# Kernel optimization log

Hardware: AMD Instinct MI355X
Metric: run time of the kernel (lower is better)

The kernel has to match this reference:

```python
import jax, jax.numpy as jnp
import numpy as np

D = 12  # grid size per axis (self.shape = [12,12,12])
BN_EPS = 1e-5


def _scatter(feats, idx, B):
    # feats: [N, C], idx: [N, 4] = (b, z, y, x). Coords are unique -> .set is exact.
    g = jnp.zeros((B, D, D, D, feats.shape[-1]), feats.dtype)
    return g.at[idx[:, 0], idx[:, 1], idx[:, 2], idx[:, 3]].set(feats)


def _subm_conv_bn_relu(feats, idx, B, W, b, gamma, beta):
    # Submanifold 3x3x3 conv == dense SAME conv on zero-filled grid, restricted
    # to the active sites (inactive neighbors contribute zero features).
    g = _scatter(feats, idx, B)  # [B, D, D, D, Cin]
    y = jax.lax.conv_general_dilated(
        g, W, window_strides=(1, 1, 1), padding='SAME',
        dimension_numbers=('NDHWC', 'DHWIO', 'NDHWC')) + b
    f = y[idx[:, 0], idx[:, 1], idx[:, 2], idx[:, 3]]  # gather active -> [N, Cout]
    # BatchNorm1d (training mode): biased batch stats over the N active points.
    mu = f.mean(axis=0)
    var = f.var(axis=0)
    f = (f - mu) * jax.lax.rsqrt(var + BN_EPS) * gamma + beta
    return jax.nn.relu(f)


def setup_inputs() -> dict:
    key = jax.random.key(0)
    B, per, Cin = 512, 864, 16
    N = B * per
    k_feat, k_coord, kp = jax.random.split(key, 3)
    # unique active voxels per batch element
    pkeys = jax.random.split(k_coord, B)
    lin = jax.vmap(lambda k: jax.random.permutation(k, D * D * D))(pkeys)[:, :per]  # [B, per]
    z, y, x = lin // (D * D), (lin // D) % D, lin % D
    bids = jnp.broadcast_to(jnp.arange(B)[:, None], (B, per))
    indices = jnp.stack([bids, z, y, x], axis=-1).reshape(N, 4).astype(jnp.int32)
    features = jax.random.normal(k_feat, (N, Cin), dtype=jnp.float32)
    ks = jax.random.split(kp, 6)
    inp = {
        'features': features, 'indices': indices, 'batch_size': B,
        'W0': jax.random.normal(ks[0], (3, 3, 3, Cin, 64), jnp.float32) * 0.05,
        'b0': jax.random.normal(ks[1], (64,), jnp.float32) * 0.05,
        'gamma0': jnp.ones((64,), jnp.float32), 'beta0': jnp.zeros((64,), jnp.float32),
        'W1': jax.random.normal(ks[2], (3, 3, 3, 64, 128), jnp.float32) * 0.05,
        'b1': jax.random.normal(ks[3], (128,), jnp.float32) * 0.05,
        'gamma1': jnp.ones((128,), jnp.float32), 'beta1': jnp.zeros((128,), jnp.float32),
        'W2': jax.random.normal(ks[4], (3, 3, 3, 128, 64), jnp.float32) * 0.05,
        'b2': jax.random.normal(ks[5], (64,), jnp.float32) * 0.05,
        'gamma2': jnp.ones((64,), jnp.float32), 'beta2': jnp.zeros((64,), jnp.float32),
    }
    return inp


def reference(features, indices, batch_size, W0, b0, gamma0, beta0,
              W1, b1, gamma1, beta1, W2, b2, gamma2, beta2):
    B = int(batch_size)
    f = _subm_conv_bn_relu(features, indices, B, W0, b0, gamma0, beta0)
    f = _subm_conv_bn_relu(f, indices, B, W1, b1, gamma1, beta1)
    f = _subm_conv_bn_relu(f, indices, B, W2, b2, gamma2, beta2)
    g = _scatter(f, indices, B)                 # [B, D, D, D, Cout]
    return jnp.transpose(g, (0, 4, 1, 2, 3))    # spconv .dense(): [B, C, D, H, W]
```

## Files before the change

### kernel.cpp

```cpp
#include <hip/hip_runtime.h>

#define DD 12
#define VOX 1728
#define BN_EPS 1e-5f
#define BATCH 512
#define PER 864
#define PERZ 865
#define NTOT (BATCH * PER)

typedef __attribute__((ext_vector_type(8))) short short8;
typedef __attribute__((ext_vector_type(4))) float f32x4;
typedef unsigned short u16;

__device__ inline u16 f2b(float f) {
    union { float f; unsigned u; } v; v.f = f;
    unsigned r = v.u + 0x7fffu + ((v.u >> 16) & 1u);
    return (u16)(r >> 16);
}
__device__ inline float b2f(u16 h) {
    union { unsigned u; float f; } v; v.u = ((unsigned)h) << 16;
    return v.f;
}
constexpr int ilog2(int v) { return v == 1 ? 0 : 1 + ilog2(v / 2); }

__device__ __forceinline__ void async_copy16(const void* g, void* l) {
    __builtin_amdgcn_global_load_lds(
        (const __attribute__((address_space(1))) void*)g,
        (__attribute__((address_space(3))) void*)l, 16, 0, 0);
}

template<int N> __device__ __forceinline__ void wait_vm() {
    if constexpr (N == 0)       asm volatile("s_waitcnt vmcnt(0)"  ::: "memory");
    else if constexpr (N == 8)  asm volatile("s_waitcnt vmcnt(8)"  ::: "memory");
    else if constexpr (N == 10) asm volatile("s_waitcnt vmcnt(10)" ::: "memory");
    else if constexpr (N == 12) asm volatile("s_waitcnt vmcnt(12)" ::: "memory");
    else if constexpr (N == 18) asm volatile("s_waitcnt vmcnt(18)" ::: "memory");
    else static_assert(N == 0, "unhandled vmcnt value");
}

__global__ void build_map_kernel(const int* __restrict__ idx, int* __restrict__ map, int N) {
    int p = blockIdx.x * blockDim.x + threadIdx.x;
    if (p >= N) return;
    const int4 v = ((const int4*)idx)[p];
    map[v.x * VOX + (v.y * DD + v.z) * DD + v.w] = p;
}

__global__ void build_nbr_kernel(const int* __restrict__ idx, const int* __restrict__ map,
                                 u16* __restrict__ nbr, int N) {
    int p = blockIdx.x * blockDim.x + threadIdx.x;
    if (p >= N) return;
    const int4 v = ((const int4*)idx)[p];
    const int base = v.x * VOX;
    const int lb = v.x * PER;
    #pragma unroll
    for (int nk = 0; nk < 27; nk++) {
        int dz = nk / 9 - 1, dy = (nk / 3) % 3 - 1, dx = nk % 3 - 1;
        int zz = v.y + dz, yy = v.z + dy, xx = v.w + dx;
        u16 out = PER;
        if (zz >= 0 && zz < DD && yy >= 0 && yy < DD && xx >= 0 && xx < DD) {
            int q = map[base + (zz * DD + yy) * DD + xx];
            if (q >= 0) out = (u16)(q - lb);
        }
        nbr[nk * N + p] = out;
    }
    #pragma unroll
    for (int nk = 27; nk < 32; nk++) nbr[nk * N + p] = PER;
}

__global__ void transpose_w_kernel(const float* __restrict__ W, u16* __restrict__ Wt,
                                   int K, int COUT, int Kpad) {
    int i = blockIdx.x * blockDim.x + threadIdx.x;
    if (i >= K * COUT) return;
    int n = i % COUT, k = i / COUT;
    Wt[(size_t)n * Kpad + k] = f2b(W[i]);
}

__global__ void cast_bf16_kernel(const float* __restrict__ in, u16* __restrict__ out, int total4) {
    int i = blockIdx.x * blockDim.x + threadIdx.x;
    if (i >= total4) return;
    int p = i >> 2, c4 = i & 3;
    int b = p / PERZ, r = p - b * PERZ;
    ushort4 o = make_ushort4(0, 0, 0, 0);
    if (r < PER) {
        float4 v = ((const float4*)in)[(size_t)(b * PER + r) * 4 + c4];
        o.x = f2b(v.x); o.y = f2b(v.y); o.z = f2b(v.z); o.w = f2b(v.w);
    }
    ((ushort4*)out)[i] = o;
}

template<int CIN, int COUT, int BM, int WM, int WN>
__global__ __launch_bounds__(256) void conv_mfma_kernel(
    const u16* __restrict__ fin, const u16* __restrict__ nbr, const u16* __restrict__ Wt,
    const float* __restrict__ bias, float* __restrict__ y, float* __restrict__ stats) {
    constexpr int Kpad   = (27 * CIN + 63) & ~63;
    constexpr int KSTEPS = Kpad / 64;
    constexpr int L2C    = ilog2(CIN);
    constexpr int BN     = WN * 64;
    constexpr int ASLOTS = BM / 32;
    constexpr int BSLOTS = BN / 32;
    constexpr int A_OFF  = BN * 128;
    constexpr int BUFB   = (BM + BN) * 128;
    static_assert(KSTEPS >= 3, "pipeline prologue needs >=3 K-steps");
    __shared__ char smem[2 * BUFB];

    const int perx = gridDim.x >> 3;
    const int bid = (blockIdx.x & 7) * perx + (blockIdx.x >> 3);
    const int p0 = bid * BM;

    const int tid = threadIdx.x;
    const int wave = tid >> 6, lane = tid & 63;
    const int wm = wave / WN, wn = wave % WN;
    const int lq = lane >> 4, lr = lane & 15;
    const int lrow = lane >> 3;
    const int kc_d = (lane & 7) ^ (lrow & 7);

    int qvoff[ASLOTS], gbase[ASLOTS];
    #pragma unroll
    for (int i = 0; i < ASLOTS; i++) {
        int m = (wave * ASLOTS + i) * 8 + lrow;
        int p = p0 + m;
        int b = p / PER;
        qvoff[i] = (((kc_d * 8) >> L2C) * NTOT + p) * 2;
        gbase[i] = b * PERZ * CIN + ((kc_d * 8) & (CIN - 1));
    }
    int bvoff[BSLOTS];
    #pragma unroll
    for (int j = 0; j < BSLOTS; j++)
        bvoff[j] = ((wave * BSLOTS + j) * 8 + lrow) * Kpad + kc_d * 8;

    int phs[2];
    phs[0] = ((0 + lq) ^ (lr & 7)) * 16;
    phs[1] = ((4 + lq) ^ (lr & 7)) * 16;
    const int aBase = A_OFF + (wm * 64 + lr) * 128;
    const int bBase = (wn * 64 + lr) * 128;

    const f32x4 fzero = {0.f, 0.f, 0.f, 0.f};
    f32x4 acc[4][4];
    #pragma unroll
    for (int i = 0; i < 4; i++)
        #pragma unroll
        for (int j = 0; j < 4; j++) acc[i][j] = fzero;

    u16 q[ASLOTS];
    auto loadQ = [&](int step) {
        int sQ = ((step * 64) >> L2C) * (NTOT * 2);
        #pragma unroll
        for (int i = 0; i < ASLOTS; i++)
            q[i] = *(const u16*)((const char*)nbr + qvoff[i] + sQ);
    };
    auto stage = [&](int step, int bo) {
        int sG = (step * 64) & (CIN - 1);
        const u16* fs = fin + sG;
        #pragma unroll
        for (int i = 0; i < ASLOTS; i++)
            async_copy16(fs + gbase[i] + ((int)q[i] << L2C),
                         smem + bo + A_OFF + (wave * ASLOTS + i) * 1024);
        const u16* wsrc = Wt + step * 64;
        #pragma unroll
        for (int j = 0; j < BSLOTS; j++)
            async_copy16(wsrc + bvoff[j], smem + bo + (wave * BSLOTS + j) * 1024);
    };

    loadQ(0);
    stage(0, 0);
    loadQ(1);

    #pragma unroll 1
    for (int kb = 0; kb < KSTEPS; kb++) {
        if (kb + 1 < KSTEPS) {
            stage(kb + 1, ((kb + 1) & 1) * BUFB);
            if (kb + 2 < KSTEPS) {
                loadQ(kb + 2);
                wait_vm<2 * ASLOTS + BSLOTS>();
            } else {
                wait_vm<ASLOTS + BSLOTS>();
            }
        } else {
            wait_vm<0>();
        }
        __builtin_amdgcn_s_barrier();

        const int so = (kb & 1) * BUFB;
        __builtin_amdgcn_s_setprio(1);
        #pragma unroll
        for (int s = 0; s < 2; s++) {
            short8 af[4], bfr[4];
            #pragma unroll
            for (int i = 0; i < 4; i++)
                af[i] = *(const short8*)(smem + so + aBase + i * 2048 + phs[s]);
            #pragma unroll
            for (int j = 0; j < 4; j++)
                bfr[j] = *(const short8*)(smem + so + bBase + j * 2048 + phs[s]);
            #pragma unroll
            for (int i = 0; i < 4; i++)
                #pragma unroll
                for (int j = 0; j < 4; j++)
                    acc[i][j] = __builtin_amdgcn_mfma_f32_16x16x32_bf16(af[i], bfr[j], acc[i][j], 0, 0, 0);
        }
        __builtin_amdgcn_s_setprio(0);
        asm volatile("s_waitcnt lgkmcnt(0)" ::: "memory");
        __builtin_amdgcn_s_barrier();
    }

    #pragma unroll
    for (int j = 0; j < 4; j++) {
        int col = wn * 64 + j * 16 + lr;
        float bv = bias[col];
        float s = 0.f, s2 = 0.f;
        #pragma unroll
        for (int i = 0; i < 4; i++) {
            int row0 = p0 + wm * 64 + i * 16 + lq * 4;
            #pragma unroll
            for (int r = 0; r < 4; r++) {
                float v = acc[i][j][r] + bv;
                y[(size_t)(row0 + r) * COUT + col] = v;
                s += v; s2 += v * v;
            }
        }
        s  += __shfl_down(s, 32);  s  += __shfl_down(s, 16);
        s2 += __shfl_down(s2, 32); s2 += __shfl_down(s2, 16);
        if (lane < 16) {
            atomicAdd(&stats[col], s);
            atomicAdd(&stats[COUT + col], s2);
        }
    }
}

template<int COUT>
__global__ void apply_kernel(const float* __restrict__ y, const float* __restrict__ stats,
                             const float* __restrict__ gamma, const float* __restrict__ beta,
                             u16* __restrict__ f, int total4) {
    int i = blockIdx.x * blockDim.x + threadIdx.x;
    if (i >= total4) return;
    constexpr int E4 = COUT / 4;
    int p = i / E4, k = i - p * E4;
    int b = p / PERZ, r = p - b * PERZ;
    int c0 = k * 4;
    const float inv_n = 1.f / (float)NTOT;
    float sc[4], sh[4];
    #pragma unroll
    for (int e = 0; e < 4; e++) {
        int c = c0 + e;
        float mu  = stats[c] * inv_n;
        float var = stats[COUT + c] * inv_n - mu * mu;
        sc[e] = gamma[c] * rsqrtf(var + BN_EPS);
        sh[e] = beta[c] - mu * sc[e];
    }
    ushort4 o = make_ushort4(0, 0, 0, 0);
    if (r < PER) {
        float4 v = ((const float4*)y)[(size_t)(b * PER + r) * E4 + k];
        float a;
        a = fmaf(v.x, sc[0], sh[0]); o.x = f2b(a > 0.f ? a : 0.f);
        a = fmaf(v.y, sc[1], sh[1]); o.y = f2b(a > 0.f ? a : 0.f);
        a = fmaf(v.z, sc[2], sh[2]); o.z = f2b(a > 0.f ? a : 0.f);
        a = fmaf(v.w, sc[3], sh[3]); o.w = f2b(a > 0.f ? a : 0.f);
    }
    ((ushort4*)f)[i] = o;
}

__global__ void output_kernel(const u16* __restrict__ f, const int* __restrict__ map,
                              float* __restrict__ out, int total) {
    int i = blockIdx.x * blockDim.x + threadIdx.x;
    if (i >= total) return;
    int voxel = i % VOX;
    int bc    = i / VOX;
    int c = bc & 63;
    int b = bc >> 6;
    int p = map[b * VOX + voxel];
    float v = 0.f;
    if (p >= 0) {
        int r = p - b * PER;
        v = b2f(f[(size_t)(b * PERZ + r) * 64 + c]);
    }
    out[i] = v;
}

__global__ void output_fused_kernel(const float* __restrict__ y, const float* __restrict__ stats,
                                    const float* __restrict__ gamma, const float* __restrict__ beta,
                                    const int* __restrict__ map, float* __restrict__ out) {
    __shared__ float tile[64][65];
    __shared__ int   prow[64];
    const int chunk = blockIdx.x;
    const int b  = chunk / (VOX / 64);
    const int v0 = (chunk % (VOX / 64)) * 64;
    const int t = threadIdx.x;
    if (t < 64) prow[t] = map[b * VOX + v0 + t];
    __syncthreads();
    const int c = t & 63;
    const float inv_n = 1.f / (float)NTOT;
    const float mu  = stats[c] * inv_n;
    const float var = stats[64 + c] * inv_n - mu * mu;
    const float sc  = gamma[c] * rsqrtf(var + BN_EPS);
    const float sh  = beta[c] - mu * sc;
    for (int v = t >> 6; v < 64; v += 4) {
        int p = prow[v];
        float val = 0.f;
        if (p >= 0) {
            float a = fmaf(y[(size_t)p * 64 + c], sc, sh);
            val = a > 0.f ? a : 0.f;
        }
        tile[v][c] = val;
    }
    __syncthreads();
    const int vv = t & 63;
    #pragma unroll
    for (int cc = t >> 6; cc < 64; cc += 4)
        out[(size_t)(b * 64 + cc) * VOX + v0 + vv] = tile[vv][cc];
}

extern "C" void kernel_launch(void* const* d_in, const int* in_sizes, int n_in,
                              void* d_out, int out_size, void* d_ws, size_t ws_size,
                              hipStream_t stream) {
    const float* feats = (const float*)d_in[0];
    const int*   idx   = (const int*)  d_in[1];
    const float* W0 = (const float*)d_in[3];
    const float* b0 = (const float*)d_in[4];
    const float* g0 = (const float*)d_in[5];
    const float* e0 = (const float*)d_in[6];
    const float* W1 = (const float*)d_in[7];
    const float* b1 = (const float*)d_in[8];
    const float* g1 = (const float*)d_in[9];
    const float* e1 = (const float*)d_in[10];
    const float* W2 = (const float*)d_in[11];
    const float* b2 = (const float*)d_in[12];
    const float* g2 = (const float*)d_in[13];
    const float* e2 = (const float*)d_in[14];

    const int N = in_sizes[0] / 16;

    char* ws = (char*)d_ws;
    size_t off = 0;
    auto alloc = [&](size_t bytes) { void* p = ws + off; off = (off + bytes + 255) & ~(size_t)255; return p; };
    int*   map   = (int*)  alloc((size_t)BATCH * VOX * 4);
    float* stats = (float*)alloc(3 * 256 * 4);
    u16*   nbr   = (u16*)  alloc((size_t)N * 32 * 2);
    u16*   wt0   = (u16*)  alloc((size_t)64  * 448  * 2);
    u16*   wt1   = (u16*)  alloc((size_t)128 * 1728 * 2);
    u16*   wt2   = (u16*)  alloc((size_t)64  * 3456 * 2);
    u16*   fbuf  = (u16*)  alloc((size_t)BATCH * PERZ * 128 * 2);
    float* y = (float*)d_out;

    const size_t y3_bytes = (size_t)N * 64 * 4;
    float* y3 = nullptr;
    if (off + y3_bytes <= ws_size) y3 = (float*)alloc(y3_bytes);

    hipMemsetAsync(map,   0xFF, (size_t)BATCH * VOX * 4, stream);
    hipMemsetAsync(stats, 0,    3 * 256 * 4, stream);
    hipMemsetAsync(wt0,   0,    (size_t)64 * 448 * 2, stream);
    build_map_kernel<<<(N + 255) / 256, 256, 0, stream>>>(idx, map, N);
    build_nbr_kernel<<<(N + 255) / 256, 256, 0, stream>>>(idx, map, nbr, N);
    transpose_w_kernel<<<(432  * 64  + 255) / 256, 256, 0, stream>>>(W0, wt0, 432,  64,  448);
    transpose_w_kernel<<<(1728 * 128 + 255) / 256, 256, 0, stream>>>(W1, wt1, 1728, 128, 1728);
    transpose_w_kernel<<<(3456 * 64  + 255) / 256, 256, 0, stream>>>(W2, wt2, 3456, 64,  3456);

    cast_bf16_kernel<<<(BATCH * PERZ * 4 + 255) / 256, 256, 0, stream>>>(feats, fbuf, BATCH * PERZ * 4);
    conv_mfma_kernel<16, 64, 256, 4, 1><<<N / 256, 256, 0, stream>>>(fbuf, nbr, wt0, b0, y, stats + 0);
    apply_kernel<64><<<(BATCH * PERZ * 16 + 255) / 256, 256, 0, stream>>>(y, stats + 0, g0, e0, fbuf, BATCH * PERZ * 16);

    conv_mfma_kernel<64, 128, 128, 2, 2><<<N / 128, 256, 0, stream>>>(fbuf, nbr, wt1, b1, y, stats + 256);
    apply_kernel<128><<<(BATCH * PERZ * 32 + 255) / 256, 256, 0, stream>>>(y, stats + 256, g1, e1, fbuf, BATCH * PERZ * 32);

    float* yL3 = y3 ? y3 : y;
    conv_mfma_kernel<128, 64, 256, 4, 1><<<N / 256, 256, 0, stream>>>(fbuf, nbr, wt2, b2, yL3, stats + 512);

    if (y3) {
        output_fused_kernel<<<BATCH * (VOX / 64), 256, 0, stream>>>(y3, stats + 512, g2, e2, map, (float*)d_out);
    } else {
        apply_kernel<64><<<(BATCH * PERZ * 16 + 255) / 256, 256, 0, stream>>>(y, stats + 512, g2, e2, fbuf, BATCH * PERZ * 16);
        output_kernel<<<(out_size + 255) / 256, 256, 0, stream>>>(fbuf, map, (float*)d_out, out_size);
    }
}
```

Before: 1.202 ms.

## Reorder active points per batch in voxel order for gather locality

Adds a per-batch compaction kernel that ranks active voxels in spatial (raster) order and rewrites the map to hold those ranks. Features are permuted into this order during the bf16 cast, and the neighbor table, output gather and fused output use rank-based indexing. Neighbor gathers in the conv kernels become spatially coherent, which should improve cache locality of feature loads. The cost is an extra small kernel and one indirect load in the cast.

```diff
diff --git a/kernel.cpp b/kernel.cpp
--- a/kernel.cpp
+++ b/kernel.cpp
@@ -45,26 +45,57 @@
     map[v.x * VOX + (v.y * DD + v.z) * DD + v.w] = p;
 }
 
-__global__ void build_nbr_kernel(const int* __restrict__ idx, const int* __restrict__ map,
+__global__ void build_sigma_kernel(int* __restrict__ map, u16* __restrict__ sig,
+                                   u16* __restrict__ voxj) {
+    const int b = blockIdx.x;
+    const int t = threadIdx.x, lane = t & 63, wave = t >> 6;
+    __shared__ int wsum[4];
+    __shared__ int base;
+    if (t == 0) base = 0;
+    __syncthreads();
+    for (int c = 0; c < 7; c++) {
+        int v = c * 256 + t;
+        int p = (v < VOX) ? map[b * VOX + v] : -1;
+        bool valid = p >= 0;
+        unsigned long long ball = __ballot(valid);
+        if (lane == 0) wsum[wave] = __popcll(ball);
+        __syncthreads();
+        int woff = 0;
+        #pragma unroll
+        for (int w = 0; w < 4; w++) if (w < wave) woff += wsum[w];
+        int rank = base + woff + __popcll(ball & ((1ull << lane) - 1ull));
+        if (valid) {
+            sig[b * PER + rank]  = (u16)(p - b * PER);
+            voxj[b * PER + rank] = (u16)v;
+            map[b * VOX + v] = rank;
+        }
+        __syncthreads();
+        if (t == 0) base += wsum[0] + wsum[1] + wsum[2] + wsum[3];
+        __syncthreads();
+    }
+}
+
+__global__ void build_nbr_kernel(const u16* __restrict__ voxj, const int* __restrict__ map,
                                  u16* __restrict__ nbr, int N) {
-    int p = blockIdx.x * blockDim.x + threadIdx.x;
-    if (p >= N) return;
-    const int4 v = ((const int4*)idx)[p];
-    const int base = v.x * VOX;
-    const int lb = v.x * PER;
+    int j = blockIdx.x * blockDim.x + threadIdx.x;
+    if (j >= N) return;
+    const int b = j / PER;
+    const int v = voxj[j];
+    const int z = v / (DD * DD), y = (v / DD) % DD, x = v % DD;
+    const int base = b * VOX;
     #pragma unroll
     for (int nk = 0; nk < 27; nk++) {
         int dz = nk / 9 - 1, dy = (nk / 3) % 3 - 1, dx = nk % 3 - 1;
-        int zz = v.y + dz, yy = v.z + dy, xx = v.w + dx;
+        int zz = z + dz, yy = y + dy, xx = x + dx;
         u16 out = PER;
         if (zz >= 0 && zz < DD && yy >= 0 && yy < DD && xx >= 0 && xx < DD) {
             int q = map[base + (zz * DD + yy) * DD + xx];
-            if (q >= 0) out = (u16)(q - lb);
-        }
-        nbr[nk * N + p] = out;
-    }
-    #pragma unroll
-    for (int nk = 27; nk < 32; nk++) nbr[nk * N + p] = PER;
+            if (q >= 0) out = (u16)q;
+        }
+        nbr[nk * N + j] = out;
+    }
+    #pragma unroll
+    for (int nk = 27; nk < 32; nk++) nbr[nk * N + j] = PER;
 }
 
 __global__ void transpose_w_kernel(const float* __restrict__ W, u16* __restrict__ Wt,
@@ -75,14 +106,16 @@
     Wt[(size_t)n * Kpad + k] = f2b(W[i]);
 }
 
-__global__ void cast_bf16_kernel(const float* __restrict__ in, u16* __restrict__ out, int total4) {
+__global__ void cast_bf16_kernel(const float* __restrict__ in, const u16* __restrict__ sig,
+                                 u16* __restrict__ out, int total4) {
     int i = blockIdx.x * blockDim.x + threadIdx.x;
     if (i >= total4) return;
     int p = i >> 2, c4 = i & 3;
     int b = p / PERZ, r = p - b * PERZ;
     ushort4 o = make_ushort4(0, 0, 0, 0);
     if (r < PER) {
-        float4 v = ((const float4*)in)[(size_t)(b * PER + r) * 4 + c4];
+        int orig = b * PER + sig[b * PER + r];
+        float4 v = ((const float4*)in)[(size_t)orig * 4 + c4];
         o.x = f2b(v.x); o.y = f2b(v.y); o.z = f2b(v.z); o.w = f2b(v.w);
     }
     ((ushort4*)out)[i] = o;
@@ -266,12 +299,9 @@
     int bc    = i / VOX;
     int c = bc & 63;
     int b = bc >> 6;
-    int p = map[b * VOX + voxel];
+    int j = map[b * VOX + voxel];
     float v = 0.f;
-    if (p >= 0) {
-        int r = p - b * PER;
-        v = b2f(f[(size_t)(b * PERZ + r) * 64 + c]);
-    }
+    if (j >= 0) v = b2f(f[(size_t)(b * PERZ + j) * 64 + c]);
     out[i] = v;
 }
 
@@ -293,10 +323,10 @@
     const float sc  = gamma[c] * rsqrtf(var + BN_EPS);
     const float sh  = beta[c] - mu * sc;
     for (int v = t >> 6; v < 64; v += 4) {
-        int p = prow[v];
+        int j = prow[v];
         float val = 0.f;
-        if (p >= 0) {
-            float a = fmaf(y[(size_t)p * 64 + c], sc, sh);
+        if (j >= 0) {
+            float a = fmaf(y[(size_t)(b * PER + j) * 64 + c], sc, sh);
             val = a > 0.f ? a : 0.f;
         }
         tile[v][c] = val;
@@ -333,6 +363,8 @@
     auto alloc = [&](size_t bytes) { void* p = ws + off; off = (off + bytes + 255) & ~(size_t)255; return p; };
     int*   map   = (int*)  alloc((size_t)BATCH * VOX * 4);
     float* stats = (float*)alloc(3 * 256 * 4);
+    u16*   sig   = (u16*)  alloc((size_t)N * 2);
+    u16*   voxj  = (u16*)  alloc((size_t)N * 2);
     u16*   nbr   = (u16*)  alloc((size_t)N * 32 * 2);
     u16*   wt0   = (u16*)  alloc((size_t)64  * 448  * 2);
     u16*   wt1   = (u16*)  alloc((size_t)128 * 1728 * 2);
@@ -348,12 +380,13 @@
     hipMemsetAsync(stats, 0,    3 * 256 * 4, stream);
     hipMemsetAsync(wt0,   0,    (size_t)64 * 448 * 2, stream);
     build_map_kernel<<<(N + 255) / 256, 256, 0, stream>>>(idx, map, N);
-    build_nbr_kernel<<<(N + 255) / 256, 256, 0, stream>>>(idx, map, nbr, N);
+    build_sigma_kernel<<<BATCH, 256, 0, stream>>>(map, sig, voxj);
+    build_nbr_kernel<<<(N + 255) / 256, 256, 0, stream>>>(voxj, map, nbr, N);
     transpose_w_kernel<<<(432  * 64  + 255) / 256, 256, 0, stream>>>(W0, wt0, 432,  64,  448);
     transpose_w_kernel<<<(1728 * 128 + 255) / 256, 256, 0, stream>>>(W1, wt1, 1728, 128, 1728);
     transpose_w_kernel<<<(3456 * 64  + 255) / 256, 256, 0, stream>>>(W2, wt2, 3456, 64,  3456);
 
-    cast_bf16_kernel<<<(BATCH * PERZ * 4 + 255) / 256, 256, 0, stream>>>(feats, fbuf, BATCH * PERZ * 4);
+    cast_bf16_kernel<<<(BATCH * PERZ * 4 + 255) / 256, 256, 0, stream>>>(feats, sig, fbuf, BATCH * PERZ * 4);
     conv_mfma_kernel<16, 64, 256, 4, 1><<<N / 256, 256, 0, stream>>>(fbuf, nbr, wt0, b0, y, stats + 0);
     apply_kernel<64><<<(BATCH * PERZ * 16 + 255) / 256, 256, 0, stream>>>(y, stats + 0, g0, e0, fbuf, BATCH * PERZ * 16);
 
```

Result: no change. 1.213 ms (+0.9%).
